# Performance work log

Measured on AMD Instinct MI355X. Metric: run time of the kernel, lower is better.

The kernel has to match this reference:

```python
import jax, jax.numpy as jnp
import numpy as np

B, N, C, H, W = 16, 10, 128, 48, 48

def setup_inputs() -> dict:
    key = jax.random.key(0)
    k0, k1 = jax.random.split(key, 2)
    x = jax.random.normal(k0, (B, N, C, H, W), dtype=jnp.float32)
    # trainable interpolation params, initialized to 0.5 as in the torch module
    pos_dec = jnp.full((N,), 0.5, dtype=jnp.float32)
    length_dec = jnp.full((N,), 0.5, dtype=jnp.float32)
    # 1x1 conv == channel-mixing matmul over N*C channels
    NC = N * C
    conv_w = jax.random.normal(k1, (NC, NC), dtype=jnp.float32) * (1.0 / np.sqrt(NC))
    conv_b = jnp.zeros((NC,), dtype=jnp.float32)
    return {"x": x, "pos_dec": pos_dec, "length_dec": length_dec,
            "conv_w": conv_w, "conv_b": conv_b}


def reference(x, pos_dec, length_dec, conv_w, conv_b):
    b, n, c, h, w = x.shape
    d = c * h * w
    q = x.reshape(b, n, d)          # proj_query (B,N,CHW)
    k = q                           # proj_key has the same flattened features
    # bi_interpolate with pos_int=i, length_int=1 reduces in closed form to:
    #   s0 = (1-pd)*K[i]   + pd*K[i+1]                      (key_short row)
    #   s1 = ld*((1-pd)*K[i+1] + pd*K[i+2])                 (zero-padded short mixed with key_long)
    # where indices wrap mod N (key was concatenated with itself).
    idx = jnp.arange(n)
    k1_ = k[:, (idx + 1) % n]       # (B,N,D)
    k2_ = k[:, (idx + 2) % n]
    pd = pos_dec[None, :, None]
    ld = length_dec[None, :, None]
    s0 = (1.0 - pd) * k + pd * k1_
    s1 = ld * ((1.0 - pd) * k1_ + pd * k2_)
    S = jnp.stack([s0, s1], axis=2)                 # (B,N,2,D) interpolated keys per group
    logits = jnp.einsum('bnd,bnkd->bnk', q, S)      # per-group 2-way attention scores
    attn = jax.nn.softmax(logits, axis=-1)          # softmax over the 2 searched keys
    out = jnp.einsum('bnk,bnkd->bnd', attn, S)      # (B,N,D)
    feat = out.reshape(b, n * c, h, w)
    conv = jnp.einsum('oc,bchw->bohw', conv_w, feat) + conv_b[None, :, None, None]
    return conv + x.reshape(b, n * c, h, w)
```

## Files before the change

### kernel.cpp

```cpp
#include <hip/hip_runtime.h>
#include <hip/hip_bf16.h>

#define BB 16
#define NN 10
#define CC 128
#define HWD 2304
#define DD (CC*HWD)
#define NC (NN*CC)

#define CH2 72
#define CHUNK2 4096

#define BM 128
#define BN 128
#define BK 32
#define TK (NC/BK)

typedef __bf16 bf16x8 __attribute__((ext_vector_type(8)));
typedef float  f32x4  __attribute__((ext_vector_type(4)));

#define FEAT_BYTES ((size_t)BB*HWD*NC*2)
#define WB_BYTES   ((size_t)NC*NC*2)
#define PART_FLOATS (BB*NN*CH2*3)

__device__ __forceinline__ ushort f2bf(float f) {
    __hip_bfloat16 h = __float2bfloat16(f);
    return *reinterpret_cast<ushort*>(&h);
}

__device__ __forceinline__ void gload_lds16(const ushort* g, ushort* l) {
    __builtin_amdgcn_global_load_lds(
        (const __attribute__((address_space(1))) void*)(const void*)g,
        (__attribute__((address_space(3))) void*)(void*)l,
        16, 0, 0);
}

__global__ __launch_bounds__(256) void k_dots(const float* __restrict__ x,
                                              float* __restrict__ part) {
    int blk = blockIdx.x;
    int ch = blk % CH2;
    int b  = blk / CH2;
    const float* base = x + (size_t)b*NN*DD + (size_t)ch*CHUNK2;
    int t = threadIdx.x;

    float4 cur[4], nxt[4], inc[4];
    #pragma unroll
    for (int i = 0; i < 4; ++i) cur[i] = *(const float4*)(base + (size_t)0*DD + i*1024 + t*4);
    #pragma unroll
    for (int i = 0; i < 4; ++i) nxt[i] = *(const float4*)(base + (size_t)1*DD + i*1024 + t*4);

    __shared__ float red[4][3];
    int w = t >> 6, l = t & 63;

    for (int n = 0; n < NN; ++n) {
        int n2 = (n + 2) % NN;
        #pragma unroll
        for (int i = 0; i < 4; ++i) inc[i] = *(const float4*)(base + (size_t)n2*DD + i*1024 + t*4);

        float s0 = 0.f, s1 = 0.f, s2 = 0.f;
        #pragma unroll
        for (int i = 0; i < 4; ++i) {
            s0 += cur[i].x*cur[i].x + cur[i].y*cur[i].y + cur[i].z*cur[i].z + cur[i].w*cur[i].w;
            s1 += cur[i].x*nxt[i].x + cur[i].y*nxt[i].y + cur[i].z*nxt[i].z + cur[i].w*nxt[i].w;
            s2 += cur[i].x*inc[i].x + cur[i].y*inc[i].y + cur[i].z*inc[i].z + cur[i].w*inc[i].w;
        }
        for (int o = 32; o > 0; o >>= 1) {
            s0 += __shfl_down(s0, o);
            s1 += __shfl_down(s1, o);
            s2 += __shfl_down(s2, o);
        }
        if (l == 0) { red[w][0] = s0; red[w][1] = s1; red[w][2] = s2; }
        __syncthreads();
        if (t == 0) {
            float r0 = 0.f, r1 = 0.f, r2 = 0.f;
            #pragma unroll
            for (int i = 0; i < 4; ++i) { r0 += red[i][0]; r1 += red[i][1]; r2 += red[i][2]; }
            float* o = part + ((size_t)(b*NN + n)*CH2 + ch)*3;
            o[0] = r0; o[1] = r1; o[2] = r2;
        }
        __syncthreads();
        #pragma unroll
        for (int i = 0; i < 4; ++i) { cur[i] = nxt[i]; nxt[i] = inc[i]; }
    }
}

__global__ void k_coef(const float* __restrict__ part,
                       const float* __restrict__ pos_dec,
                       const float* __restrict__ len_dec,
                       float* __restrict__ coef) {
    int bn = threadIdx.x;
    if (bn >= BB*NN) return;
    int n = bn % NN;
    float d0 = 0.f, d1 = 0.f, d2 = 0.f;
    const float* p = part + (size_t)bn*CH2*3;
    for (int i = 0; i < CH2; ++i) { d0 += p[i*3]; d1 += p[i*3+1]; d2 += p[i*3+2]; }
    float pd = pos_dec[n], ld = len_dec[n];
    float l0 = (1.f - pd)*d0 + pd*d1;
    float l1 = ld*((1.f - pd)*d1 + pd*d2);
    float m  = fmaxf(l0, l1);
    float e0 = expf(l0 - m), e1 = expf(l1 - m);
    float inv = 1.f/(e0 + e1);
    float a0 = e0*inv, a1 = e1*inv;
    coef[bn*3+0] = a0*(1.f - pd);
    coef[bn*3+1] = a0*pd + a1*ld*(1.f - pd);
    coef[bn*3+2] = a1*ld*pd;
}

__global__ __launch_bounds__(256) void k_wconv(const float* __restrict__ w,
                                               ushort* __restrict__ wb) {
    int i = blockIdx.x*blockDim.x + threadIdx.x;
    size_t idx = (size_t)i*4;
    if (idx >= (size_t)NC*NC) return;
    float4 a = *(const float4*)(w + idx);
    ushort4 o;
    o.x = f2bf(a.x); o.y = f2bf(a.y); o.z = f2bf(a.z); o.w = f2bf(a.w);
    *(ushort4*)(wb + idx) = o;
}

__global__ __launch_bounds__(256) void k_feat(const float* __restrict__ x,
                                              const float* __restrict__ coef,
                                              ushort* __restrict__ featT) {
    __shared__ float tile[32*129];
    int hwt = blockIdx.x;
    int n   = blockIdx.y;
    int b   = blockIdx.z;
    int bn  = b*NN + n;
    float c0 = coef[bn*3+0], c1 = coef[bn*3+1], c2 = coef[bn*3+2];
    int n1 = (n + 1) % NN, n2 = (n + 2) % NN;
    const float* p0 = x + ((size_t)b*NN + n )*DD;
    const float* p1 = x + ((size_t)b*NN + n1)*DD;
    const float* p2 = x + ((size_t)b*NN + n2)*DD;
    int t = threadIdx.x;
    int hw0 = hwt*32;

    int ccl = t >> 3;
    int hwi = (t & 7) * 4;
    #pragma unroll
    for (int p = 0; p < 4; ++p) {
        int cc = p*32 + ccl;
        size_t off = (size_t)cc*HWD + hw0 + hwi;
        float4 a = *(const float4*)(p0 + off);
        float4 u = *(const float4*)(p1 + off);
        float4 v = *(const float4*)(p2 + off);
        tile[(hwi+0)*129 + cc] = c0*a.x + c1*u.x + c2*v.x;
        tile[(hwi+1)*129 + cc] = c0*a.y + c1*u.y + c2*v.y;
        tile[(hwi+2)*129 + cc] = c0*a.z + c1*u.z + c2*v.z;
        tile[(hwi+3)*129 + cc] = c0*a.w + c1*u.w + c2*v.w;
    }
    __syncthreads();

    int hwl = t >> 4;
    int cc0 = (t & 15) * 8;
    #pragma unroll
    for (int p = 0; p < 2; ++p) {
        int hw = p*16 + hwl;
        const float* src = &tile[hw*129 + cc0];
        union { ushort us[8]; uint4 v; } pk;
        #pragma unroll
        for (int j = 0; j < 8; ++j) pk.us[j] = f2bf(src[j]);
        ushort* dst = featT + (size_t)b*HWD*NC + (size_t)(hw0 + hw)*NC + n*CC + cc0;
        *(uint4*)dst = pk.v;
    }
}

__global__ __launch_bounds__(256, 4) void k_gemm(const ushort* __restrict__ Wb,
                                                 const ushort* __restrict__ featT,
                                                 const float* __restrict__ bias,
                                                 const float* __restrict__ x,
                                                 float* __restrict__ out) {
    __shared__ ushort As[BM*BK];
    __shared__ ushort Bs[BN*BK];

    int bid = blockIdx.x;
    int wkid = (bid & 7) * 360 + (bid >> 3);
    int b    = wkid / 180;
    int rem  = wkid % 180;
    int hwt  = rem / 10;
    int ot   = rem % 10;
    int o0 = ot*BM, hw0 = hwt*BN;

    int t = threadIdx.x;
    int l = t & 63;
    int w = t >> 6;
    int wr = w >> 1, wc = w & 1;

    const ushort* Ag = Wb + (size_t)o0*NC;
    const ushort* Bg = featT + (size_t)b*HWD*NC + (size_t)hw0*NC;

    int r0 = t >> 2, c0 = t & 3;
    size_t g0 = (size_t)r0*NC + (size_t)((c0 ^ ((r0 >> 1) & 3)) * 8);
    size_t g1 = g0 + (size_t)64*NC;

    int fr = l & 15;
    int fc = l >> 4;

    f32x4 acc[4][4] = {};

    for (int kt = 0; kt < TK; ++kt) {
        size_t k0 = (size_t)kt*BK;
        __syncthreads();
        gload_lds16(Ag + g0 + k0, As + t*8);
        gload_lds16(Ag + g1 + k0, As + (256 + t)*8);
        gload_lds16(Bg + g0 + k0, Bs + t*8);
        gload_lds16(Bg + g1 + k0, Bs + (256 + t)*8);
        __syncthreads();

        bf16x8 afr[4], bfr[4];
        #pragma unroll
        for (int m = 0; m < 4; ++m) {
            int row = wr*64 + m*16 + fr;
            afr[m] = *(const bf16x8*)&As[row*BK + ((fc ^ ((row >> 1) & 3))*8)];
        }
        #pragma unroll
        for (int n = 0; n < 4; ++n) {
            int row = wc*64 + n*16 + fr;
            bfr[n] = *(const bf16x8*)&Bs[row*BK + ((fc ^ ((row >> 1) & 3))*8)];
        }
        #pragma unroll
        for (int m = 0; m < 4; ++m)
            #pragma unroll
            for (int n = 0; n < 4; ++n)
                acc[m][n] = __builtin_amdgcn_mfma_f32_16x16x32_bf16(afr[m], bfr[n], acc[m][n], 0, 0, 0);
    }

    #pragma unroll
    for (int m = 0; m < 4; ++m) {
        int ro_base = o0 + wr*64 + m*16 + ((l >> 4) << 2);
        #pragma unroll
        for (int n = 0; n < 4; ++n) {
            int col = hw0 + wc*64 + n*16 + (l & 15);
            #pragma unroll
            for (int r = 0; r < 4; ++r) {
                int ro = ro_base + r;
                size_t idx = (size_t)b*NC*HWD + (size_t)ro*HWD + col;
                out[idx] = acc[m][n][r] + bias[ro] + x[idx];
            }
        }
    }
}

extern "C" void kernel_launch(void* const* d_in, const int* in_sizes, int n_in,
                              void* d_out, int out_size, void* d_ws, size_t ws_size,
                              hipStream_t stream) {
    const float* x       = (const float*)d_in[0];
    const float* pos_dec = (const float*)d_in[1];
    const float* len_dec = (const float*)d_in[2];
    const float* conv_w  = (const float*)d_in[3];
    const float* conv_b  = (const float*)d_in[4];
    float* out = (float*)d_out;

    char* ws = (char*)d_ws;
    ushort* featT = (ushort*)ws;
    ushort* wb    = (ushort*)(ws + FEAT_BYTES);
    float*  part  = (float*)(ws + FEAT_BYTES + WB_BYTES);
    float*  coef  = part + PART_FLOATS;

    k_dots <<<dim3(BB*CH2), 256, 0, stream>>>(x, part);
    k_coef <<<dim3(1), 256, 0, stream>>>(part, pos_dec, len_dec, coef);
    k_wconv<<<dim3(1600), 256, 0, stream>>>(conv_w, wb);
    k_feat <<<dim3(72, NN, BB), 256, 0, stream>>>(x, coef, featT);
    k_gemm <<<dim3(2880), 256, 0, stream>>>(wb, featT, conv_b, x, out);
}
```

Baseline: 315.0 us.

## Double-buffer GEMM LDS tiles and reuse x slices across groups in feat kernel

```diff
diff --git a/kernel.cpp b/kernel.cpp
--- a/kernel.cpp
+++ b/kernel.cpp
@@ -122,44 +122,61 @@
                                               ushort* __restrict__ featT) {
     __shared__ float tile[32*129];
     int hwt = blockIdx.x;
-    int n   = blockIdx.y;
-    int b   = blockIdx.z;
-    int bn  = b*NN + n;
-    float c0 = coef[bn*3+0], c1 = coef[bn*3+1], c2 = coef[bn*3+2];
-    int n1 = (n + 1) % NN, n2 = (n + 2) % NN;
-    const float* p0 = x + ((size_t)b*NN + n )*DD;
-    const float* p1 = x + ((size_t)b*NN + n1)*DD;
-    const float* p2 = x + ((size_t)b*NN + n2)*DD;
+    int b   = blockIdx.y;
     int t = threadIdx.x;
     int hw0 = hwt*32;
-
-    int ccl = t >> 3;
-    int hwi = (t & 7) * 4;
-    #pragma unroll
-    for (int p = 0; p < 4; ++p) {
-        int cc = p*32 + ccl;
-        size_t off = (size_t)cc*HWD + hw0 + hwi;
-        float4 a = *(const float4*)(p0 + off);
-        float4 u = *(const float4*)(p1 + off);
-        float4 v = *(const float4*)(p2 + off);
-        tile[(hwi+0)*129 + cc] = c0*a.x + c1*u.x + c2*v.x;
-        tile[(hwi+1)*129 + cc] = c0*a.y + c1*u.y + c2*v.y;
-        tile[(hwi+2)*129 + cc] = c0*a.z + c1*u.z + c2*v.z;
-        tile[(hwi+3)*129 + cc] = c0*a.w + c1*u.w + c2*v.w;
-    }
-    __syncthreads();
-
-    int hwl = t >> 4;
-    int cc0 = (t & 15) * 8;
-    #pragma unroll
-    for (int p = 0; p < 2; ++p) {
-        int hw = p*16 + hwl;
-        const float* src = &tile[hw*129 + cc0];
-        union { ushort us[8]; uint4 v; } pk;
-        #pragma unroll
-        for (int j = 0; j < 8; ++j) pk.us[j] = f2bf(src[j]);
-        ushort* dst = featT + (size_t)b*HWD*NC + (size_t)(hw0 + hw)*NC + n*CC + cc0;
-        *(uint4*)dst = pk.v;
+    const float* xb = x + (size_t)b*NN*DD;
+
+    int c_[4], ch_[4];
+    size_t off_[4];
+    #pragma unroll
+    for (int i = 0; i < 4; ++i) {
+        int s = i*256 + t;
+        c_[i] = s >> 3; ch_[i] = s & 7;
+        off_[i] = (size_t)c_[i]*HWD + hw0 + ch_[i]*4;
+    }
+
+    float4 s0[4], s1[4], s2[4], s3[4];
+    #pragma unroll
+    for (int i = 0; i < 4; ++i) s0[i] = *(const float4*)(xb + (size_t)0*DD + off_[i]);
+    #pragma unroll
+    for (int i = 0; i < 4; ++i) s1[i] = *(const float4*)(xb + (size_t)1*DD + off_[i]);
+    #pragma unroll
+    for (int i = 0; i < 4; ++i) s2[i] = *(const float4*)(xb + (size_t)2*DD + off_[i]);
+
+    for (int n = 0; n < NN; ++n) {
+        int n3 = (n + 3) % NN;
+        #pragma unroll
+        for (int i = 0; i < 4; ++i) s3[i] = *(const float4*)(xb + (size_t)n3*DD + off_[i]);
+
+        int bn = b*NN + n;
+        float c0 = coef[bn*3+0], c1 = coef[bn*3+1], c2 = coef[bn*3+2];
+
+        #pragma unroll
+        for (int i = 0; i < 4; ++i) {
+            int hwb = ch_[i]*4, cc = c_[i];
+            tile[(hwb+0)*129 + cc] = c0*s0[i].x + c1*s1[i].x + c2*s2[i].x;
+            tile[(hwb+1)*129 + cc] = c0*s0[i].y + c1*s1[i].y + c2*s2[i].y;
+            tile[(hwb+2)*129 + cc] = c0*s0[i].z + c1*s1[i].z + c2*s2[i].z;
+            tile[(hwb+3)*129 + cc] = c0*s0[i].w + c1*s1[i].w + c2*s2[i].w;
+        }
+        __syncthreads();
+
+        int hwl = t >> 4;
+        int cc0 = (t & 15) * 8;
+        #pragma unroll
+        for (int p = 0; p < 2; ++p) {
+            int hw = p*16 + hwl;
+            const float* src = &tile[hw*129 + cc0];
+            union { ushort us[8]; uint4 v; } pk;
+            #pragma unroll
+            for (int j = 0; j < 8; ++j) pk.us[j] = f2bf(src[j]);
+            ushort* dst = featT + (size_t)b*HWD*NC + (size_t)(hw0 + hw)*NC + n*CC + cc0;
+            *(uint4*)dst = pk.v;
+        }
+        __syncthreads();
+        #pragma unroll
+        for (int i = 0; i < 4; ++i) { s0[i] = s1[i]; s1[i] = s2[i]; s2[i] = s3[i]; }
     }
 }
 
@@ -168,8 +185,8 @@
                                                  const float* __restrict__ bias,
                                                  const float* __restrict__ x,
                                                  float* __restrict__ out) {
-    __shared__ ushort As[BM*BK];
-    __shared__ ushort Bs[BN*BK];
+    __shared__ ushort As[2][BM*BK];
+    __shared__ ushort Bs[2][BN*BK];
 
     int bid = blockIdx.x;
     int wkid = (bid & 7) * 360 + (bid >> 3);
@@ -191,37 +208,52 @@
     size_t g0 = (size_t)r0*NC + (size_t)((c0 ^ ((r0 >> 1) & 3)) * 8);
     size_t g1 = g0 + (size_t)64*NC;
 
+#define STAGE(buf_, kt_) do { \
+    size_t k0_ = (size_t)(kt_)*BK; \
+    ushort* da_ = &As[buf_][0]; \
+    ushort* db_ = &Bs[buf_][0]; \
+    gload_lds16(Ag + g0 + k0_, da_ + t*8); \
+    gload_lds16(Ag + g1 + k0_, da_ + (256 + t)*8); \
+    gload_lds16(Bg + g0 + k0_, db_ + t*8); \
+    gload_lds16(Bg + g1 + k0_, db_ + (256 + t)*8); \
+} while (0)
+
     int fr = l & 15;
     int fc = l >> 4;
 
     f32x4 acc[4][4] = {};
 
+    STAGE(0, 0);
+    __syncthreads();
+
     for (int kt = 0; kt < TK; ++kt) {
-        size_t k0 = (size_t)kt*BK;
-        __syncthreads();
-        gload_lds16(Ag + g0 + k0, As + t*8);
-        gload_lds16(Ag + g1 + k0, As + (256 + t)*8);
-        gload_lds16(Bg + g0 + k0, Bs + t*8);
-        gload_lds16(Bg + g1 + k0, Bs + (256 + t)*8);
-        __syncthreads();
+        int buf = kt & 1;
+        if (kt + 1 < TK) STAGE(buf ^ 1, kt + 1);
+        __builtin_amdgcn_sched_barrier(0);
+
+        const ushort* as = &As[buf][0];
+        const ushort* bs = &Bs[buf][0];
 
         bf16x8 afr[4], bfr[4];
         #pragma unroll
         for (int m = 0; m < 4; ++m) {
             int row = wr*64 + m*16 + fr;
-            afr[m] = *(const bf16x8*)&As[row*BK + ((fc ^ ((row >> 1) & 3))*8)];
+            afr[m] = *(const bf16x8*)&as[row*BK + ((fc ^ ((row >> 1) & 3))*8)];
         }
         #pragma unroll
         for (int n = 0; n < 4; ++n) {
             int row = wc*64 + n*16 + fr;
-            bfr[n] = *(const bf16x8*)&Bs[row*BK + ((fc ^ ((row >> 1) & 3))*8)];
+            bfr[n] = *(const bf16x8*)&bs[row*BK + ((fc ^ ((row >> 1) & 3))*8)];
         }
         #pragma unroll
         for (int m = 0; m < 4; ++m)
             #pragma unroll
             for (int n = 0; n < 4; ++n)
                 acc[m][n] = __builtin_amdgcn_mfma_f32_16x16x32_bf16(afr[m], bfr[n], acc[m][n], 0, 0, 0);
-    }
+
+        __syncthreads();
+    }
+#undef STAGE
 
     #pragma unroll
     for (int m = 0; m < 4; ++m) {
@@ -258,6 +290,6 @@
     k_dots <<<dim3(BB*CH2), 256, 0, stream>>>(x, part);
     k_coef <<<dim3(1), 256, 0, stream>>>(part, pos_dec, len_dec, coef);
     k_wconv<<<dim3(1600), 256, 0, stream>>>(conv_w, wb);
-    k_feat <<<dim3(72, NN, BB), 256, 0, stream>>>(x, coef, featT);
+    k_feat <<<dim3(72, BB), 256, 0, stream>>>(x, coef, featT);
     k_gemm <<<dim3(2880), 256, 0, stream>>>(wb, featT, conv_b, x, out);
 }
```

Result: no change. 314.5 us (-0.2%).
